# Kernel optimization log

Measured on AMD Instinct MI355X. Metric: run time of the kernel, lower is better.

Reference implementation:

```python
import jax, jax.numpy as jnp
import numpy as np

B, L, H, S = 16, 2048, 1024, 32
P, N_ASP, N_RAT = 256, 8, 5


def _layernorm(x, scale, bias, eps=1e-5):
    mu = jnp.mean(x, axis=-1, keepdims=True)
    var = jnp.mean(jnp.square(x - mu), axis=-1, keepdims=True)
    return (x - mu) * jax.lax.rsqrt(var + eps) * scale + bias


def _bndl(x, ln_s, ln_b, W):
    # BnDropLin eval: LayerNorm -> (Dropout off) -> Linear(no bias)
    return _layernorm(x, ln_s, ln_b) @ W


def setup_inputs() -> dict:
    key = jax.random.key(0)
    ks = jax.random.split(key, 8)
    outputs = jax.random.normal(ks[0], (B, L, H), dtype=jnp.float32)
    mask = jnp.ones((B, L), dtype=jnp.float32)
    # p_index: binary sentence-boundary markers, exactly S per doc, min gap 2
    rng = np.random.default_rng(0)
    p = np.zeros((B, L), dtype=np.int32)
    for b in range(B):
        idx = np.sort(rng.choice(L // 2 - 1, size=S, replace=False)) * 2 + 1
        p[b, idx] = 1
    p_index = jnp.asarray(p)
    sc = 0.02
    params = dict(
        ln_a_s=jnp.ones((H,), jnp.float32), ln_a_b=jnp.zeros((H,), jnp.float32),
        W_a=jax.random.normal(ks[1], (H, P), jnp.float32) * sc,
        ln_s_s=jnp.ones((H,), jnp.float32), ln_s_b=jnp.zeros((H,), jnp.float32),
        W_s=jax.random.normal(ks[2], (H, P), jnp.float32) * sc,
        ln_asp_s=jnp.ones((P,), jnp.float32), ln_asp_b=jnp.zeros((P,), jnp.float32),
        W_asp=jax.random.normal(ks[3], (P, N_ASP + 1), jnp.float32) * sc,
        ln_se_s=jnp.ones((P,), jnp.float32), ln_se_b=jnp.zeros((P,), jnp.float32),
        W_se=jax.random.normal(ks[4], (P, N_RAT), jnp.float32) * sc,
    )
    return dict(outputs=outputs, mask=mask, p_index=p_index, n_sent=S, **params)


def _segment_means(proj, end, start):
    # proj: [B, L, P]; start/end: [B, S] token index ranges [start, end)
    c = jnp.concatenate([jnp.zeros_like(proj[:, :1]), jnp.cumsum(proj, axis=1)], axis=1)  # [B,L+1,P]
    s_end = jnp.take_along_axis(c, end[:, :, None], axis=1)
    s_beg = jnp.take_along_axis(c, start[:, :, None], axis=1)
    cnt = (end - start).astype(proj.dtype)[:, :, None]
    return (s_end - s_beg) / cnt  # [B, S, P]


def reference(outputs, mask, p_index, n_sent,
              ln_a_s, ln_a_b, W_a, ln_s_s, ln_s_b, W_s,
              ln_asp_s, ln_asp_b, W_asp, ln_se_s, ln_se_b, W_se):
    b, l, h = outputs.shape
    n_asp = W_asp.shape[1] - 1
    flat = outputs.reshape(-1, h)
    a_proj = jax.nn.gelu(_bndl(flat, ln_a_s, ln_a_b, W_a), approximate=False).reshape(b, l, -1)
    s_proj = jax.nn.gelu(_bndl(flat, ln_s_s, ln_s_b, W_s), approximate=False).reshape(b, l, -1)
    # sentence boundaries: positions of nonzeros (exactly n_sent per row)
    pos = jnp.where(p_index > 0, jnp.arange(l)[None, :], l)
    pi = jnp.sort(pos, axis=1)[:, :n_sent]                      # [B,S] boundary idx (exclusive end)
    start = jnp.concatenate([jnp.zeros_like(pi[:, :1]), pi[:, :-1] + 1], axis=1)
    a_sent = _segment_means(a_proj, pi, start)                  # [B,S,P]
    s_sent = _segment_means(s_proj, pi, start)                  # [B,S,P]
    a_flat = a_sent.reshape(b * n_sent, -1)
    s_flat = s_sent.reshape(b * n_sent, -1)
    aspect_dist = jax.nn.softmax(_bndl(a_flat, ln_asp_s, ln_asp_b, W_asp), axis=1)  # [N, n_asp+1]
    aw = aspect_dist[:, :n_asp]                                 # [N, n_asp]
    sent_bmm = aw[:, :, None] * s_flat[:, None, :]              # [N, n_asp, P]
    doc_sum = sent_bmm.reshape(b, n_sent, n_asp, -1).sum(axis=1)        # [B, n_asp, P]
    w_sum = aw.reshape(b, n_sent, n_asp).sum(axis=1)[:, :, None]        # [B, n_asp, 1]
    doc_emb = doc_sum / w_sum
    # shared sentiment head (ModuleList([m]*n_asp) aliases one module)
    result = _bndl(doc_emb, ln_se_s, ln_se_b, W_se)             # [B, n_asp, n_rat]
    aspect_doc = aspect_dist.reshape(b, n_sent, n_asp + 1)
    return (result, outputs, aspect_doc)
```

## Files before the change

### kernel.cpp

```cpp
#include <hip/hip_runtime.h>
#include <cstdint>
#include <cstddef>

#define B_   16
#define L_   2048
#define H_   1024
#define S_   32
#define P_   256
#define NASP 8
#define NRAT 5
#define M_   (B_*L_)
#define N_   (2*P_)

typedef unsigned short u16;
typedef __bf16 bf16;
typedef u16  u16x4  __attribute__((ext_vector_type(4)));
typedef u16  u16x8  __attribute__((ext_vector_type(8)));
typedef bf16 bf16x8 __attribute__((ext_vector_type(8)));
typedef float f32x4 __attribute__((ext_vector_type(4)));

__device__ __forceinline__ u16 f2b(float f){
  unsigned int u = __float_as_uint(f);
  u += 0x7FFFu + ((u >> 16) & 1u);
  return (u16)(u >> 16);
}
__device__ __forceinline__ float b2f(u16 v){
  return __uint_as_float(((unsigned int)v) << 16);
}

__device__ __forceinline__ void gload_lds16(const u16* g, u16* l){
  __builtin_amdgcn_global_load_lds(
      (const __attribute__((address_space(1))) unsigned int*)g,
      (__attribute__((address_space(3))) unsigned int*)l, 16, 0, 0);
}

__device__ __forceinline__ float2 block_reduce2(float a, float b){
  __shared__ float sh[8];
  #pragma unroll
  for (int o = 32; o > 0; o >>= 1){
    a += __shfl_down(a, o, 64);
    b += __shfl_down(b, o, 64);
  }
  int w = threadIdx.x >> 6;
  if ((threadIdx.x & 63) == 0){ sh[w] = a; sh[w + 4] = b; }
  __syncthreads();
  float2 r;
  r.x = sh[0] + sh[1] + sh[2] + sh[3];
  r.y = sh[4] + sh[5] + sh[6] + sh[7];
  __syncthreads();
  return r;
}

__global__ void fold_k(const float* __restrict__ Wa, const float* __restrict__ Ws,
                       const float* __restrict__ sa, const float* __restrict__ ba,
                       const float* __restrict__ ss, const float* __restrict__ bs,
                       u16* __restrict__ WcT, float* __restrict__ biasc){
  int n = blockIdx.x;
  const float* W; const float* sc; const float* bi; int col;
  if (n < P_){ W = Wa; sc = sa; bi = ba; col = n; }
  else       { W = Ws; sc = ss; bi = bs; col = n - P_; }
  float bacc = 0.f;
  #pragma unroll
  for (int i = 0; i < 4; ++i){
    int k = threadIdx.x + i * 256;
    float w = W[(size_t)k * P_ + col];
    WcT[(size_t)n * H_ + k] = f2b(w * sc[k]);
    bacc += w * bi[k];
  }
  float2 r = block_reduce2(bacc, 0.f);
  if (threadIdx.x == 0) biasc[n] = r.x;
}

__global__ void markers_k(const int* __restrict__ p_index, int* __restrict__ pi){
  int b = blockIdx.x;
  int lane = threadIdx.x;
  int cnt = 0;
  for (int c = 0; c < L_ / 64; ++c){
    int pos = c * 64 + lane;
    bool f = p_index[(size_t)b * L_ + pos] > 0;
    unsigned long long m = __ballot(f);
    int before = __popcll(m & ((1ull << lane) - 1ull));
    if (f){
      int idx = cnt + before;
      if (idx < S_) pi[b * S_ + idx] = pos;
    }
    cnt += __popcll(m);
  }
}

__global__ void stats_xhat_k(const float* __restrict__ x, u16* __restrict__ xhat){
  int row = blockIdx.x;
  int t = threadIdx.x;
  float4 v = ((const float4*)(x + (size_t)row * H_))[t];
  float s  = v.x + v.y + v.z + v.w;
  float ss = v.x*v.x + v.y*v.y + v.z*v.z + v.w*v.w;
  float2 r = block_reduce2(s, ss);
  float mean = r.x * (1.f / H_);
  float var  = fmaxf(r.y * (1.f / H_) - mean * mean, 0.f);
  float rstd = rsqrtf(var + 1e-5f);
  u16x4 o;
  o[0] = f2b((v.x - mean) * rstd);
  o[1] = f2b((v.y - mean) * rstd);
  o[2] = f2b((v.z - mean) * rstd);
  o[3] = f2b((v.w - mean) * rstd);
  ((u16x4*)(xhat + (size_t)row * H_))[t] = o;
}

__global__ __launch_bounds__(256) void gemm_k(const u16* __restrict__ xhat,
                                              const u16* __restrict__ WcT,
                                              const float* __restrict__ biasc,
                                              u16* __restrict__ proj){
  __shared__ __align__(16) u16 As[128 * 32];
  __shared__ __align__(16) u16 Bs[128 * 32];
  int t = threadIdx.x;
  unsigned int l = blockIdx.x;
  unsigned int xcd  = l & 7;
  unsigned int slot = l >> 3;
  int nbase = (int)(slot & 3) * 128;
  int mbase = (int)(xcd * 32 + (slot >> 2)) * 128;

  int w = t >> 6, lane = t & 63;
  int wr = w >> 1, wc = w & 1;
  int quad = lane >> 4, l15 = lane & 15;

  int g = (lane & 3) ^ ((lane >> 3) & 3);
  int r0 = (w * 2 + 0) * 16 + (lane >> 2);
  int r1 = (w * 2 + 1) * 16 + (lane >> 2);
  const u16* gA0 = xhat + (size_t)(mbase + r0) * H_ + g * 8;
  const u16* gA1 = xhat + (size_t)(mbase + r1) * H_ + g * 8;
  const u16* gB0 = WcT  + (size_t)(nbase + r0) * H_ + g * 8;
  const u16* gB1 = WcT  + (size_t)(nbase + r1) * H_ + g * 8;
  u16* lA0 = As + (w * 2 + 0) * 512;
  u16* lA1 = As + (w * 2 + 1) * 512;
  u16* lB0 = Bs + (w * 2 + 0) * 512;
  u16* lB1 = Bs + (w * 2 + 1) * 512;

  f32x4 acc[4][4] = {};

  for (int kk = 0; kk < H_; kk += 32){
    __syncthreads();
    gload_lds16(gA0 + kk, lA0);
    gload_lds16(gA1 + kk, lA1);
    gload_lds16(gB0 + kk, lB0);
    gload_lds16(gB1 + kk, lB1);
    __syncthreads();

    bf16x8 af[4], bfr[4];
    #pragma unroll
    for (int im = 0; im < 4; ++im){
      int R = wr * 64 + im * 16 + l15;
      int cq = quad ^ ((R >> 1) & 3);
      af[im] = *reinterpret_cast<const bf16x8*>(&As[R * 32 + cq * 8]);
    }
    #pragma unroll
    for (int in = 0; in < 4; ++in){
      int R = wc * 64 + in * 16 + l15;
      int cq = quad ^ ((R >> 1) & 3);
      bfr[in] = *reinterpret_cast<const bf16x8*>(&Bs[R * 32 + cq * 8]);
    }
    #pragma unroll
    for (int im = 0; im < 4; ++im)
      #pragma unroll
      for (int in = 0; in < 4; ++in)
        acc[im][in] = __builtin_amdgcn_mfma_f32_16x16x32_bf16(af[im], bfr[in], acc[im][in], 0, 0, 0);
  }

  #pragma unroll
  for (int in = 0; in < 4; ++in){
    int col = nbase + wc * 64 + in * 16 + l15;
    float bv = biasc[col];
    #pragma unroll
    for (int im = 0; im < 4; ++im){
      #pragma unroll
      for (int r = 0; r < 4; ++r){
        int rowg = mbase + wr * 64 + im * 16 + quad * 4 + r;
        float vv = acc[im][in][r] + bv;
        float gl = 0.5f * vv * (1.0f + erff(vv * 0.70710678118654752f));
        proj[(size_t)rowg * N_ + col] = f2b(gl);
      }
    }
  }
}

__global__ __launch_bounds__(1024) void segmean_k(const u16* __restrict__ proj,
                                                  const int* __restrict__ pi,
                                                  float* __restrict__ sent){
  int b = blockIdx.x, j = blockIdx.y;
  int t = threadIdx.x;
  int rg   = t >> 6;
  int lane = t & 63;
  int end   = pi[b * S_ + j];
  int start = (j == 0) ? 0 : (pi[b * S_ + j - 1] + 1);
  end   = min(max(end, 0), L_);
  start = min(max(start, 0), end);
  int cnt = max(end - start, 1);
  float inv = 1.0f / (float)cnt;

  float s[8] = {};
  const u16* base = proj + ((size_t)b * L_ + start) * N_ + lane * 8;
  for (int r = rg; r < cnt; r += 16){
    u16x8 v = *reinterpret_cast<const u16x8*>(base + (size_t)r * N_);
    #pragma unroll
    for (int k = 0; k < 8; ++k) s[k] += b2f(v[k]);
  }

  __shared__ float sh[16][N_];
  #pragma unroll
  for (int k = 0; k < 8; ++k) sh[rg][lane * 8 + k] = s[k];
  __syncthreads();

  if (t < N_){
    float acc = 0.f;
    #pragma unroll
    for (int g = 0; g < 16; ++g) acc += sh[g][t];
    sent[((size_t)b * S_ + j) * N_ + t] = acc * inv;
  }
}

__global__ void aspect_k(const float* __restrict__ sent,
                         const float* __restrict__ lns, const float* __restrict__ lnb,
                         const float* __restrict__ Wasp,
                         float* __restrict__ out_adoc, float* __restrict__ aw){
  int sidx = blockIdx.x;
  int t = threadIdx.x;
  float a = sent[(size_t)sidx * N_ + t];
  float2 r = block_reduce2(a, a * a);
  float mean = r.x * (1.f / P_);
  float var  = fmaxf(r.y * (1.f / P_) - mean * mean, 0.f);
  float rstd = rsqrtf(var + 1e-5f);
  __shared__ float shv[P_];
  shv[t] = (a - mean) * rstd * lns[t] + lnb[t];
  __syncthreads();
  __shared__ float lg[NASP + 1];
  if (t < NASP + 1){
    float acc = 0.f;
    for (int p = 0; p < P_; ++p) acc += shv[p] * Wasp[p * (NASP + 1) + t];
    lg[t] = acc;
  }
  __syncthreads();
  __shared__ float pr[NASP + 1];
  if (t == 0){
    float m = lg[0];
    #pragma unroll
    for (int i = 1; i < NASP + 1; ++i) m = fmaxf(m, lg[i]);
    float s = 0.f;
    #pragma unroll
    for (int i = 0; i < NASP + 1; ++i){ float e = expf(lg[i] - m); pr[i] = e; s += e; }
    float is = 1.f / s;
    #pragma unroll
    for (int i = 0; i < NASP + 1; ++i) pr[i] *= is;
  }
  __syncthreads();
  if (t < NASP + 1) out_adoc[(size_t)sidx * (NASP + 1) + t] = pr[t];
  if (t < NASP)     aw[(size_t)sidx * NASP + t] = pr[t];
}

__global__ void result_k(const float* __restrict__ sent, const float* __restrict__ aw,
                         const float* __restrict__ lns, const float* __restrict__ lnb,
                         const float* __restrict__ Wse, float* __restrict__ out){
  int ba = blockIdx.x;
  int b = ba >> 3, a = ba & 7;
  int t = threadIdx.x;
  float acc = 0.f, wsum = 0.f;
  for (int s2 = 0; s2 < S_; ++s2){
    float w = aw[((size_t)(b * S_ + s2)) * NASP + a];
    acc  += w * sent[((size_t)(b * S_ + s2)) * N_ + P_ + t];
    wsum += w;
  }
  float d = acc / fmaxf(wsum, 1e-20f);
  float2 r = block_reduce2(d, d * d);
  float mean = r.x * (1.f / P_);
  float var  = fmaxf(r.y * (1.f / P_) - mean * mean, 0.f);
  float rstd = rsqrtf(var + 1e-5f);
  __shared__ float shv[P_];
  shv[t] = (d - mean) * rstd * lns[t] + lnb[t];
  __syncthreads();
  if (t < NRAT){
    float s = 0.f;
    for (int p = 0; p < P_; ++p) s += shv[p] * Wse[p * NRAT + t];
    out[(size_t)ba * NRAT + t] = s;
  }
}

__global__ void copy_k(const float4* __restrict__ src, float4* __restrict__ dst){
  size_t i = (size_t)blockIdx.x * 256 + threadIdx.x;
  dst[i] = src[i];
}

extern "C" void kernel_launch(void* const* d_in, const int* in_sizes, int n_in,
                              void* d_out, int out_size, void* d_ws, size_t ws_size,
                              hipStream_t stream) {
  const float* x        = (const float*)d_in[0];
  const int*   p_index  = (const int*)d_in[2];
  const float* ln_a_s   = (const float*)d_in[4];
  const float* ln_a_b   = (const float*)d_in[5];
  const float* W_a      = (const float*)d_in[6];
  const float* ln_s_s   = (const float*)d_in[7];
  const float* ln_s_b   = (const float*)d_in[8];
  const float* W_s      = (const float*)d_in[9];
  const float* ln_asp_s = (const float*)d_in[10];
  const float* ln_asp_b = (const float*)d_in[11];
  const float* W_asp    = (const float*)d_in[12];
  const float* ln_se_s  = (const float*)d_in[13];
  const float* ln_se_b  = (const float*)d_in[14];
  const float* W_se     = (const float*)d_in[15];

  float* out_result = (float*)d_out;
  float* out_echo   = out_result + 640;
  float* out_adoc   = out_echo + (size_t)M_ * H_;

  u16* proj = (u16*)out_echo;
  u16* xhat = proj + (size_t)M_ * N_;

  char* ws = (char*)d_ws;
  u16*   WcT   = (u16*)ws;   ws += (size_t)N_ * H_ * 2;
  float* biasc = (float*)ws; ws += (size_t)N_ * 4;
  int*   pi    = (int*)ws;   ws += (size_t)B_ * S_ * 4;
  float* sent  = (float*)ws; ws += (size_t)B_ * S_ * N_ * 4;
  float* aw    = (float*)ws; ws += (size_t)B_ * S_ * NASP * 4;

  fold_k<<<N_, 256, 0, stream>>>(W_a, W_s, ln_a_s, ln_a_b, ln_s_s, ln_s_b, WcT, biasc);
  markers_k<<<B_, 64, 0, stream>>>(p_index, pi);
  stats_xhat_k<<<M_, 256, 0, stream>>>(x, xhat);
  gemm_k<<<1024, 256, 0, stream>>>(xhat, WcT, biasc, proj);
  segmean_k<<<dim3(B_, S_), 1024, 0, stream>>>(proj, pi, sent);
  aspect_k<<<B_ * S_, 256, 0, stream>>>(sent, ln_asp_s, ln_asp_b, W_asp, out_adoc, aw);
  result_k<<<B_ * NASP, 256, 0, stream>>>(sent, aw, ln_se_s, ln_se_b, W_se, out_result);
  copy_k<<<(M_ * H_ / 4) / 256, 256, 0, stream>>>((const float4*)x, (float4*)out_echo);
}
```

Measured before the change: 405.9 us.

## Fuse echo copy into normalization pass and double-buffer GEMM LDS tiles

```diff
diff --git a/kernel.cpp b/kernel.cpp
--- a/kernel.cpp
+++ b/kernel.cpp
@@ -88,10 +88,13 @@
   }
 }
 
-__global__ void stats_xhat_k(const float* __restrict__ x, u16* __restrict__ xhat){
+template<bool FUSE_ECHO>
+__global__ void stats_xhat_k(const float* __restrict__ x, u16* __restrict__ xhat,
+                             float4* __restrict__ echo){
   int row = blockIdx.x;
   int t = threadIdx.x;
   float4 v = ((const float4*)(x + (size_t)row * H_))[t];
+  if (FUSE_ECHO) echo[(size_t)row * (H_ / 4) + t] = v;
   float s  = v.x + v.y + v.z + v.w;
   float ss = v.x*v.x + v.y*v.y + v.z*v.z + v.w*v.w;
   float2 r = block_reduce2(s, ss);
@@ -110,8 +113,8 @@
                                               const u16* __restrict__ WcT,
                                               const float* __restrict__ biasc,
                                               u16* __restrict__ proj){
-  __shared__ __align__(16) u16 As[128 * 32];
-  __shared__ __align__(16) u16 Bs[128 * 32];
+  __shared__ __align__(16) u16 As[2 * 128 * 32];
+  __shared__ __align__(16) u16 Bs[2 * 128 * 32];
   int t = threadIdx.x;
   unsigned int l = blockIdx.x;
   unsigned int xcd  = l & 7;
@@ -130,40 +133,50 @@
   const u16* gA1 = xhat + (size_t)(mbase + r1) * H_ + g * 8;
   const u16* gB0 = WcT  + (size_t)(nbase + r0) * H_ + g * 8;
   const u16* gB1 = WcT  + (size_t)(nbase + r1) * H_ + g * 8;
-  u16* lA0 = As + (w * 2 + 0) * 512;
-  u16* lA1 = As + (w * 2 + 1) * 512;
-  u16* lB0 = Bs + (w * 2 + 0) * 512;
-  u16* lB1 = Bs + (w * 2 + 1) * 512;
 
   f32x4 acc[4][4] = {};
 
-  for (int kk = 0; kk < H_; kk += 32){
-    __syncthreads();
-    gload_lds16(gA0 + kk, lA0);
-    gload_lds16(gA1 + kk, lA1);
-    gload_lds16(gB0 + kk, lB0);
-    gload_lds16(gB1 + kk, lB1);
-    __syncthreads();
-
+  auto stage = [&](int bb, int kk){
+    u16* a = As + bb * 4096 + (w * 2) * 512;
+    u16* b = Bs + bb * 4096 + (w * 2) * 512;
+    gload_lds16(gA0 + kk, a);
+    gload_lds16(gA1 + kk, a + 512);
+    gload_lds16(gB0 + kk, b);
+    gload_lds16(gB1 + kk, b + 512);
+  };
+  auto compute = [&](int bb){
+    const u16* ab = As + bb * 4096;
+    const u16* bb_ = Bs + bb * 4096;
     bf16x8 af[4], bfr[4];
     #pragma unroll
     for (int im = 0; im < 4; ++im){
       int R = wr * 64 + im * 16 + l15;
       int cq = quad ^ ((R >> 1) & 3);
-      af[im] = *reinterpret_cast<const bf16x8*>(&As[R * 32 + cq * 8]);
+      af[im] = *reinterpret_cast<const bf16x8*>(&ab[R * 32 + cq * 8]);
     }
     #pragma unroll
     for (int in = 0; in < 4; ++in){
       int R = wc * 64 + in * 16 + l15;
       int cq = quad ^ ((R >> 1) & 3);
-      bfr[in] = *reinterpret_cast<const bf16x8*>(&Bs[R * 32 + cq * 8]);
+      bfr[in] = *reinterpret_cast<const bf16x8*>(&bb_[R * 32 + cq * 8]);
     }
     #pragma unroll
     for (int im = 0; im < 4; ++im)
       #pragma unroll
       for (int in = 0; in < 4; ++in)
         acc[im][in] = __builtin_amdgcn_mfma_f32_16x16x32_bf16(af[im], bfr[in], acc[im][in], 0, 0, 0);
-  }
+  };
+
+  stage(0, 0);
+  __syncthreads();
+  int cur = 0;
+  for (int step = 0; step < 31; ++step){
+    stage(cur ^ 1, (step + 1) * 32);
+    compute(cur);
+    __syncthreads();
+    cur ^= 1;
+  }
+  compute(cur);
 
   #pragma unroll
   for (int in = 0; in < 4; ++in){
@@ -309,9 +322,6 @@
   float* out_echo   = out_result + 640;
   float* out_adoc   = out_echo + (size_t)M_ * H_;
 
-  u16* proj = (u16*)out_echo;
-  u16* xhat = proj + (size_t)M_ * N_;
-
   char* ws = (char*)d_ws;
   u16*   WcT   = (u16*)ws;   ws += (size_t)N_ * H_ * 2;
   float* biasc = (float*)ws; ws += (size_t)N_ * 4;
@@ -319,12 +329,29 @@
   float* sent  = (float*)ws; ws += (size_t)B_ * S_ * N_ * 4;
   float* aw    = (float*)ws; ws += (size_t)B_ * S_ * NASP * 4;
 
+  size_t small_used = (size_t)(ws - (char*)d_ws);
+  size_t big_need   = small_used + (size_t)M_ * N_ * 2 + (size_t)M_ * H_ * 2;
+  bool   big_ws     = ws_size >= big_need;
+
+  u16* proj; u16* xhat;
+  if (big_ws){
+    proj = (u16*)ws;
+    xhat = proj + (size_t)M_ * N_;
+  } else {
+    proj = (u16*)out_echo;
+    xhat = proj + (size_t)M_ * N_;
+  }
+
   fold_k<<<N_, 256, 0, stream>>>(W_a, W_s, ln_a_s, ln_a_b, ln_s_s, ln_s_b, WcT, biasc);
   markers_k<<<B_, 64, 0, stream>>>(p_index, pi);
-  stats_xhat_k<<<M_, 256, 0, stream>>>(x, xhat);
+  if (big_ws)
+    stats_xhat_k<true ><<<M_, 256, 0, stream>>>(x, xhat, (float4*)out_echo);
+  else
+    stats_xhat_k<false><<<M_, 256, 0, stream>>>(x, xhat, nullptr);
   gemm_k<<<1024, 256, 0, stream>>>(xhat, WcT, biasc, proj);
   segmean_k<<<dim3(B_, S_), 1024, 0, stream>>>(proj, pi, sent);
   aspect_k<<<B_ * S_, 256, 0, stream>>>(sent, ln_asp_s, ln_asp_b, W_asp, out_adoc, aw);
   result_k<<<B_ * NASP, 256, 0, stream>>>(sent, aw, ln_se_s, ln_se_b, W_se, out_result);
-  copy_k<<<(M_ * H_ / 4) / 256, 256, 0, stream>>>((const float4*)x, (float4*)out_echo);
-}
+  if (!big_ws)
+    copy_k<<<(M_ * H_ / 4) / 256, 256, 0, stream>>>((const float4*)x, (float4*)out_echo);
+}
```

Result: no change. 412.9 us (+1.7%).
